# Performance work log

Hardware: AMD Instinct MI355X
Metric: run time of the kernel (lower is better)

The kernel has to match this reference:

```python
import jax, jax.numpy as jnp
import numpy as np

NPOINT = 1024
NSAMPLE = 32
BN_EPS = 1e-5


def setup_inputs() -> dict:
    key = jax.random.key(0)
    ks = jax.random.split(key, 8)
    B, N, C = 16, 4096, 64
    chans = [C + 3, 64, 64, 128]
    d = {
        "xyz": jax.random.normal(ks[0], (B, N, 3), jnp.float32),
        "points": jax.random.normal(ks[1], (B, N, C), jnp.float32),
    }
    for i in range(3):
        d[f"w{i+1}"] = jax.random.normal(ks[2 + i], (chans[i + 1], chans[i]), jnp.float32) / np.sqrt(chans[i]).astype(np.float32)
        d[f"b{i+1}"] = jnp.zeros((chans[i + 1],), jnp.float32)
        d[f"g{i+1}"] = jnp.ones((chans[i + 1],), jnp.float32)
        d[f"be{i+1}"] = jnp.zeros((chans[i + 1],), jnp.float32)
    return d


def farthest_point_sample(xyz, npoint):
    # xyz: [B, N, 3] -> centroids: [B, npoint] int32 (deterministic start at index 0)
    B, N, _ = xyz.shape

    def step(carry, _):
        distance, farthest = carry
        centroid = jnp.take_along_axis(xyz, farthest[:, None, None], axis=1)  # [B,1,3]
        dist = jnp.sum((xyz - centroid) ** 2, axis=-1)                         # [B,N]
        distance = jnp.minimum(distance, dist)
        new_far = jnp.argmax(distance, axis=-1).astype(jnp.int32)
        return (distance, new_far), farthest

    init = (jnp.full((B, N), 1e10, xyz.dtype), jnp.zeros((B,), jnp.int32))
    _, cents = jax.lax.scan(step, init, None, length=npoint)  # [npoint, B]
    return cents.T  # [B, npoint]


def index_points(points, idx):
    # points: [B,N,C], idx: [B,...] -> [B,...,C]
    return jax.vmap(lambda p, i: p[i])(points, idx)


def bn_relu(h, g, be):
    # training-mode BatchNorm over all axes except channel (last), biased var
    m = h.mean(axis=(0, 1, 2), keepdims=True)
    v = h.var(axis=(0, 1, 2), keepdims=True)
    return jax.nn.relu((h - m) / jnp.sqrt(v + BN_EPS) * g + be)


def reference(xyz, points, w1, b1, g1, be1, w2, b2, g2, be2, w3, b3, g3, be3):
    # --- sample_and_group ---
    fps_idx = farthest_point_sample(xyz, NPOINT)           # [B,S]
    new_xyz = index_points(xyz, fps_idx)                   # [B,S,3]
    # query_ball_point in source ignores radius: kNN via argsort of sq dists
    sqrdists = jnp.sum((new_xyz[:, :, None, :] - xyz[:, None, :, :]) ** 2, axis=-1)  # [B,S,N]
    _, group_idx = jax.lax.top_k(-sqrdists, NSAMPLE)       # [B,S,K] smallest distances
    grouped_xyz = index_points(xyz, group_idx) - new_xyz[:, :, None, :]  # [B,S,K,3]
    grouped_pts = index_points(points, group_idx)          # [B,S,K,C]
    new_points = jnp.concatenate([grouped_xyz, grouped_pts], axis=-1)    # [B,S,K,C+3]
    # --- shared MLP (1x1 conv + BN + ReLU) x3, channel-last layout ---
    h = bn_relu(jnp.einsum("bskc,oc->bsko", new_points, w1) + b1, g1, be1)
    h = bn_relu(jnp.einsum("bskc,oc->bsko", h, w2) + b2, g2, be2)
    h = bn_relu(jnp.einsum("bskc,oc->bsko", h, w3) + b3, g3, be3)
    # max-pool over the neighbor (nsample) axis
    out = jnp.max(h, axis=2)  # [B,S,128]
    return (new_xyz, out)
```

## Files before the change

### kernel.cpp

```cpp
#include <hip/hip_runtime.h>
#include <cstdint>

#define NB   16
#define NPT  4096
#define CINP 64
#define SP   1024
#define KNB  32
#define NROWS (NB*SP*KNB)
#define NT_F  524288.0f
#define NBLK12 4096
#define NBLK3  8192

typedef float v2f __attribute__((ext_vector_type(2)));

__device__ __forceinline__ float sqdist3(float ax, float ay, float az,
                                         float bx, float by, float bz) {
  float dx = ax - bx, dy = ay - by, dz = az - bz;
  return __fadd_rn(__fadd_rn(__fmul_rn(dx, dx), __fmul_rn(dy, dy)), __fmul_rn(dz, dz));
}

#define DPP_STAGE_MAXF(v, ctrl)                                                   \
  do {                                                                            \
    int _t = __builtin_amdgcn_update_dpp(0, __float_as_int(v), ctrl, 0xf, 0xf, false); \
    v = fmaxf(v, __int_as_float(_t));                                             \
  } while (0)

__device__ __forceinline__ float wave_max_f32(float v) {
  DPP_STAGE_MAXF(v, 0x111);
  DPP_STAGE_MAXF(v, 0x112);
  DPP_STAGE_MAXF(v, 0x114);
  DPP_STAGE_MAXF(v, 0x118);
  DPP_STAGE_MAXF(v, 0x142);
  DPP_STAGE_MAXF(v, 0x143);
  return __int_as_float(__builtin_amdgcn_readlane(__float_as_int(v), 63));
}

#define DPP_STAGE_MINU(v, ctrl)                                                   \
  do {                                                                            \
    unsigned _t = (unsigned)__builtin_amdgcn_update_dpp(                          \
        (int)0xFFFFFFFF, (int)(v), ctrl, 0xf, 0xf, false);                        \
    v = (v < _t) ? v : _t;                                                        \
  } while (0)

__device__ __forceinline__ unsigned wave_min_u32(unsigned v) {
  DPP_STAGE_MINU(v, 0x111);
  DPP_STAGE_MINU(v, 0x112);
  DPP_STAGE_MINU(v, 0x114);
  DPP_STAGE_MINU(v, 0x118);
  DPP_STAGE_MINU(v, 0x142);
  DPP_STAGE_MINU(v, 0x143);
  return (unsigned)__builtin_amdgcn_readlane((int)v, 63);
}

#define DPP_STAGE_ADDI(v, ctrl)                                                   \
  do {                                                                            \
    int _t = __builtin_amdgcn_update_dpp(0, (v), ctrl, 0xf, 0xf, false);          \
    v += _t;                                                                      \
  } while (0)

__device__ __forceinline__ int wave_sum_i32(int v) {
  DPP_STAGE_ADDI(v, 0x111);
  DPP_STAGE_ADDI(v, 0x112);
  DPP_STAGE_ADDI(v, 0x114);
  DPP_STAGE_ADDI(v, 0x118);
  DPP_STAGE_ADDI(v, 0x142);
  DPP_STAGE_ADDI(v, 0x143);
  return __builtin_amdgcn_readlane(v, 63);
}

__global__ __launch_bounds__(256) void fps_kernel(const float* __restrict__ xyz,
                                                  float* __restrict__ newxyz) {
#pragma clang fp contract(off)
  const int b = blockIdx.x, t = threadIdx.x;
  __shared__ __align__(16) float s4[NPT * 4];
  __shared__ unsigned long long s_red[2][4];
  const float* gx = xyz + b * NPT * 3;
  for (int i = t; i < NPT * 3; i += 256) s4[(i / 3) * 4 + (i % 3)] = gx[i];
  __syncthreads();
  v2f px[8], py[8], pz[8], dst[8];
#pragma unroll
  for (int k = 0; k < 8; ++k) {
    float4 a = *(const float4*)&s4[(t + (2 * k) * 256) * 4];
    float4 c = *(const float4*)&s4[(t + (2 * k + 1) * 256) * 4];
    px[k].x = a.x; px[k].y = c.x;
    py[k].x = a.y; py[k].y = c.y;
    pz[k].x = a.z; pz[k].y = c.z;
    dst[k].x = 1e10f; dst[k].y = 1e10f;
  }
  float cx = s4[0], cy = s4[1], cz = s4[2];
  const int w = t >> 6;
  int buf = 0;
  for (int it = 0; it < SP; ++it) {
    if (t == 0) {
      float* o = newxyz + (b * SP + it) * 3;
      o[0] = cx; o[1] = cy; o[2] = cz;
    }
    v2f vcx; vcx.x = cx; vcx.y = cx;
    v2f vcy; vcy.x = cy; vcy.y = cy;
    v2f vcz; vcz.x = cz; vcz.y = cz;
    float bd = -1.0f; int bi = 0;
#pragma unroll
    for (int k = 0; k < 8; ++k) {
      v2f dx = px[k] - vcx;
      v2f dy = py[k] - vcy;
      v2f dz = pz[k] - vcz;
      v2f dd = (dx * dx + dy * dy) + dz * dz;
      float n0 = fminf(dst[k].x, dd.x);
      float n1 = fminf(dst[k].y, dd.y);
      dst[k].x = n0; dst[k].y = n1;
      if (n0 > bd) { bd = n0; bi = t + (2 * k) * 256; }
      if (n1 > bd) { bd = n1; bi = t + (2 * k + 1) * 256; }
    }
    float dw = wave_max_f32(bd);
    unsigned cand = (bd == dw) ? (unsigned)bi : 0xFFFFFFFFu;
    unsigned iw = wave_min_u32(cand);
    if ((t & 63) == 0)
      s_red[buf][w] = ((unsigned long long)__float_as_uint(dw) << 32) | (4095u - iw);
    __syncthreads();
    unsigned long long k0 = s_red[buf][0], k1 = s_red[buf][1];
    unsigned long long k2 = s_red[buf][2], k3 = s_red[buf][3];
    unsigned long long ka = k0 > k1 ? k0 : k1;
    unsigned long long kb = k2 > k3 ? k2 : k3;
    unsigned long long km = ka > kb ? ka : kb;
    int p = 4095 - (int)(km & 0xFFFFFFFFull);
    float4 cc = *(const float4*)&s4[p * 4];
    cx = cc.x; cy = cc.y; cz = cc.z;
    buf ^= 1;
  }
}

__global__ __launch_bounds__(256) void knn_kernel(const float* __restrict__ xyz,
                                                  const float* __restrict__ newxyz,
                                                  int* __restrict__ gidx) {
  const int t = threadIdx.x, lane = t & 63, w = t >> 6;
  const int q = blockIdx.x * 4 + w;
  const int b = q >> 10;
  const float* nx = newxyz + q * 3;
  const float qx = nx[0], qy = nx[1], qz = nx[2];
  const float* xb = xyz + b * NPT * 3;
  float d[64];
#pragma unroll
  for (int j = 0; j < 64; ++j) {
    int p = j * 64 + lane;
    d[j] = sqdist3(xb[p * 3], xb[p * 3 + 1], xb[p * 3 + 2], qx, qy, qz);
  }
  unsigned V = 0;
  for (int bit = 30; bit >= 0; --bit) {
    unsigned cand = V | (1u << bit);
    int c = 0;
#pragma unroll
    for (int j = 0; j < 64; ++j) c += (__float_as_uint(d[j]) < cand) ? 1 : 0;
    int ct = wave_sum_i32(c);
    if (ct < KNB) V = cand;
  }
  __shared__ int s_cnt[4], s_eqcnt[4], s_eq[4][64];
  if (lane == 0) { s_cnt[w] = 0; s_eqcnt[w] = 0; }
  __syncthreads();
  int* gout = gidx + q * KNB;
#pragma unroll
  for (int j = 0; j < 64; ++j) {
    unsigned db = __float_as_uint(d[j]);
    if (db < V) {
      int pos = atomicAdd(&s_cnt[w], 1);
      if (pos < KNB) gout[pos] = j * 64 + lane;
    } else if (db == V) {
      int pos = atomicAdd(&s_eqcnt[w], 1);
      if (pos < 64) s_eq[w][pos] = j * 64 + lane;
    }
  }
  __syncthreads();
  if (lane == 0) {
    int c1 = s_cnt[w]; if (c1 > KNB) c1 = KNB;
    int ne = s_eqcnt[w]; if (ne > 64) ne = 64;
    int need = KNB - c1;
    for (int m = 0; m < need; ++m) {
      int bi = -1, bv = 0x7fffffff;
      for (int e = 0; e < ne; ++e) {
        int v = s_eq[w][e];
        if (v < bv) { bv = v; bi = e; }
      }
      gout[c1 + m] = bv;
      if (bi >= 0) s_eq[w][bi] = 0x7fffffff;
    }
  }
}

__global__ __launch_bounds__(256) void layer1_kernel(
    const float* __restrict__ xyz, const float* __restrict__ points,
    const float* __restrict__ newxyz, const int* __restrict__ gidx,
    const float* __restrict__ w1, const float* __restrict__ b1,
    float* __restrict__ h1, float* __restrict__ part) {
  const int t = threadIdx.x, blk = blockIdx.x;
  const int R0 = blk * 128;
  const int b = R0 >> 15;
  __shared__ __align__(16) float xs[67][132];
  __shared__ __align__(16) float wsm[67][68];
  __shared__ float red[2][32][64];
  {
    int o = t & 63;
    for (int c = t >> 6; c < 67; c += 4) wsm[c][o] = w1[o * 67 + c];
  }
  {
    int r = t >> 1, q = t & 1;
    int R = R0 + r;
    int idx = gidx[R];
    if (q == 0) {
      const float* xp = xyz + (size_t)(b * NPT + idx) * 3;
      const float* nq = newxyz + (size_t)(R >> 5) * 3;
      xs[0][r] = xp[0] - nq[0];
      xs[1][r] = xp[1] - nq[1];
      xs[2][r] = xp[2] - nq[2];
    }
    const float* pp = points + (size_t)(b * NPT + idx) * CINP + q * 32;
#pragma unroll
    for (int i = 0; i < 8; ++i) {
      float4 v = *(const float4*)(pp + i * 4);
      int c = 3 + q * 32 + i * 4;
      xs[c][r] = v.x; xs[c + 1][r] = v.y; xs[c + 2][r] = v.z; xs[c + 3][r] = v.w;
    }
  }
  __syncthreads();
  const int tr = t & 31, to = t >> 5;
  float acc[4][8];
#pragma unroll
  for (int j = 0; j < 8; ++j) {
    float bb = b1[to * 8 + j];
#pragma unroll
    for (int i = 0; i < 4; ++i) acc[i][j] = bb;
  }
  for (int c = 0; c < 67; ++c) {
    float4 xv = *(const float4*)&xs[c][tr * 4];
    float4 w0 = *(const float4*)&wsm[c][to * 8];
    float4 w1v = *(const float4*)&wsm[c][to * 8 + 4];
    float xa[4] = {xv.x, xv.y, xv.z, xv.w};
    float wa[8] = {w0.x, w0.y, w0.z, w0.w, w1v.x, w1v.y, w1v.z, w1v.w};
#pragma unroll
    for (int i = 0; i < 4; ++i)
#pragma unroll
      for (int j = 0; j < 8; ++j) acc[i][j] += xa[i] * wa[j];
  }
#pragma unroll
  for (int i = 0; i < 4; ++i) {
    float4 s0; s0.x = acc[i][0]; s0.y = acc[i][1]; s0.z = acc[i][2]; s0.w = acc[i][3];
    float4 s1; s1.x = acc[i][4]; s1.y = acc[i][5]; s1.z = acc[i][6]; s1.w = acc[i][7];
    float* hp = &h1[(size_t)(R0 + tr * 4 + i) * 64 + to * 8];
    *(float4*)hp = s0;
    *(float4*)(hp + 4) = s1;
  }
#pragma unroll
  for (int j = 0; j < 8; ++j) {
    float s1 = acc[0][j] + acc[1][j] + acc[2][j] + acc[3][j];
    float s2 = acc[0][j] * acc[0][j] + acc[1][j] * acc[1][j] +
               acc[2][j] * acc[2][j] + acc[3][j] * acc[3][j];
    red[0][tr][to * 8 + j] = s1;
    red[1][tr][to * 8 + j] = s2;
  }
  __syncthreads();
  if (t < 128) {
    int stat = t >> 6, o = t & 63;
    float v = 0.f;
#pragma unroll
    for (int k = 0; k < 32; ++k) v += red[stat][k][o];
    part[(size_t)(stat * 64 + o) * NBLK12 + blk] = v;
  }
}

__global__ __launch_bounds__(256) void layer2_kernel(
    const float* __restrict__ hin, const float* __restrict__ bn,
    const float* __restrict__ w2, const float* __restrict__ b2,
    float* __restrict__ hout, float* __restrict__ part) {
  const int t = threadIdx.x, blk = blockIdx.x;
  const size_t R0 = (size_t)blk * 128;
  __shared__ __align__(16) float xs[64][132];
  __shared__ __align__(16) float wsm[64][68];
  __shared__ float red[2][32][64];
  {
    int o = t & 63;
    for (int c = t >> 6; c < 64; c += 4) wsm[c][o] = w2[o * 64 + c];
  }
  {
    int r = t >> 1, q = t & 1;
    const float* hp = hin + (R0 + r) * 64 + q * 32;
#pragma unroll
    for (int i = 0; i < 8; ++i) {
      int c = q * 32 + i * 4;
      float4 v = *(const float4*)(hp + i * 4);
      float4 sc = *(const float4*)(bn + c);
      float4 sh = *(const float4*)(bn + 64 + c);
      xs[c][r]     = fmaxf(v.x * sc.x + sh.x, 0.f);
      xs[c + 1][r] = fmaxf(v.y * sc.y + sh.y, 0.f);
      xs[c + 2][r] = fmaxf(v.z * sc.z + sh.z, 0.f);
      xs[c + 3][r] = fmaxf(v.w * sc.w + sh.w, 0.f);
    }
  }
  __syncthreads();
  const int tr = t & 31, to = t >> 5;
  float acc[4][8];
#pragma unroll
  for (int j = 0; j < 8; ++j) {
    float bb = b2[to * 8 + j];
#pragma unroll
    for (int i = 0; i < 4; ++i) acc[i][j] = bb;
  }
  for (int c = 0; c < 64; ++c) {
    float4 xv = *(const float4*)&xs[c][tr * 4];
    float4 w0 = *(const float4*)&wsm[c][to * 8];
    float4 w1v = *(const float4*)&wsm[c][to * 8 + 4];
    float xa[4] = {xv.x, xv.y, xv.z, xv.w};
    float wa[8] = {w0.x, w0.y, w0.z, w0.w, w1v.x, w1v.y, w1v.z, w1v.w};
#pragma unroll
    for (int i = 0; i < 4; ++i)
#pragma unroll
      for (int j = 0; j < 8; ++j) acc[i][j] += xa[i] * wa[j];
  }
#pragma unroll
  for (int i = 0; i < 4; ++i) {
    float4 s0; s0.x = acc[i][0]; s0.y = acc[i][1]; s0.z = acc[i][2]; s0.w = acc[i][3];
    float4 s1; s1.x = acc[i][4]; s1.y = acc[i][5]; s1.z = acc[i][6]; s1.w = acc[i][7];
    float* hp = &hout[(R0 + tr * 4 + i) * 64 + to * 8];
    *(float4*)hp = s0;
    *(float4*)(hp + 4) = s1;
  }
#pragma unroll
  for (int j = 0; j < 8; ++j) {
    float s1 = acc[0][j] + acc[1][j] + acc[2][j] + acc[3][j];
    float s2 = acc[0][j] * acc[0][j] + acc[1][j] * acc[1][j] +
               acc[2][j] * acc[2][j] + acc[3][j] * acc[3][j];
    red[0][tr][to * 8 + j] = s1;
    red[1][tr][to * 8 + j] = s2;
  }
  __syncthreads();
  if (t < 128) {
    int stat = t >> 6, o = t & 63;
    float v = 0.f;
#pragma unroll
    for (int k = 0; k < 32; ++k) v += red[stat][k][o];
    part[(size_t)(stat * 64 + o) * NBLK12 + blk] = v;
  }
}

__global__ __launch_bounds__(256) void layer3_kernel(
    const float* __restrict__ hin, const float* __restrict__ bn,
    const float* __restrict__ w3, const float* __restrict__ b3,
    float* __restrict__ maxh, float* __restrict__ minh, float* __restrict__ part) {
  const int t = threadIdx.x, blk = blockIdx.x;
  const size_t R0 = (size_t)blk * 64;
  __shared__ __align__(16) float smem[64 * 68 + 64 * 136];
  float* xs = smem;
  float* wsm = smem + 64 * 68;
  {
    int o = t & 127, q = t >> 7;
    for (int c = q; c < 64; c += 2) wsm[c * 136 + o] = w3[o * 64 + c];
  }
  {
    int r = t >> 2, q = t & 3;
    const float* hp = hin + (R0 + r) * 64 + q * 16;
#pragma unroll
    for (int i = 0; i < 4; ++i) {
      int c = q * 16 + i * 4;
      float4 v = *(const float4*)(hp + i * 4);
      float4 sc = *(const float4*)(bn + c);
      float4 sh = *(const float4*)(bn + 64 + c);
      xs[c * 68 + r]       = fmaxf(v.x * sc.x + sh.x, 0.f);
      xs[(c + 1) * 68 + r] = fmaxf(v.y * sc.y + sh.y, 0.f);
      xs[(c + 2) * 68 + r] = fmaxf(v.z * sc.z + sh.z, 0.f);
      xs[(c + 3) * 68 + r] = fmaxf(v.w * sc.w + sh.w, 0.f);
    }
  }
  __syncthreads();
  const int tr = t & 15, to = t >> 4;
  float acc[4][8];
#pragma unroll
  for (int j = 0; j < 8; ++j) {
    float bb = b3[to * 8 + j];
#pragma unroll
    for (int i = 0; i < 4; ++i) acc[i][j] = bb;
  }
  for (int c = 0; c < 64; ++c) {
    float4 xv = *(const float4*)&xs[c * 68 + tr * 4];
    float4 wv0 = *(const float4*)&wsm[c * 136 + to * 8];
    float4 wv1 = *(const float4*)&wsm[c * 136 + to * 8 + 4];
    float xa[4] = {xv.x, xv.y, xv.z, xv.w};
    float wa[8] = {wv0.x, wv0.y, wv0.z, wv0.w, wv1.x, wv1.y, wv1.z, wv1.w};
#pragma unroll
    for (int i = 0; i < 4; ++i)
#pragma unroll
      for (int j = 0; j < 8; ++j) acc[i][j] += xa[i] * wa[j];
  }
  __syncthreads();
  float* red = smem;
#pragma unroll
  for (int j = 0; j < 8; ++j) {
    float s1 = acc[0][j] + acc[1][j] + acc[2][j] + acc[3][j];
    float s2 = acc[0][j] * acc[0][j] + acc[1][j] * acc[1][j] +
               acc[2][j] * acc[2][j] + acc[3][j] * acc[3][j];
    red[(0 * 16 + tr) * 128 + to * 8 + j] = s1;
    red[(1 * 16 + tr) * 128 + to * 8 + j] = s2;
  }
  __syncthreads();
  {
    int stat = t >> 7, o = t & 127;
    float v = 0.f;
#pragma unroll
    for (int k = 0; k < 16; ++k) v += red[(stat * 16 + k) * 128 + o];
    part[(size_t)(stat * 128 + o) * NBLK3 + blk] = v;
  }
  __syncthreads();
#pragma unroll
  for (int j = 0; j < 8; ++j) {
    float mx = fmaxf(fmaxf(acc[0][j], acc[1][j]), fmaxf(acc[2][j], acc[3][j]));
    float mn = fminf(fminf(acc[0][j], acc[1][j]), fminf(acc[2][j], acc[3][j]));
    red[(0 * 16 + tr) * 128 + to * 8 + j] = mx;
    red[(1 * 16 + tr) * 128 + to * 8 + j] = mn;
  }
  __syncthreads();
  {
    int g = t >> 7, o = t & 127;
    float mx = -1e30f, mn = 1e30f;
#pragma unroll
    for (int k = 0; k < 8; ++k) {
      mx = fmaxf(mx, red[(0 * 16 + g * 8 + k) * 128 + o]);
      mn = fminf(mn, red[(1 * 16 + g * 8 + k) * 128 + o]);
    }
    size_t bs = (size_t)blk * 2 + g;
    maxh[bs * 128 + o] = mx;
    minh[bs * 128 + o] = mn;
  }
}

__global__ __launch_bounds__(256) void bn_finalize(const float* __restrict__ part,
                                                   const float* __restrict__ g,
                                                   const float* __restrict__ be,
                                                   float* __restrict__ bnout,
                                                   int Cout, int nblk) {
  const int o = blockIdx.x, t = threadIdx.x;
  float s1 = 0.f, s2 = 0.f;
  const float* p1 = part + (size_t)o * nblk;
  const float* p2 = part + (size_t)(Cout + o) * nblk;
  for (int i = t; i < nblk; i += 256) { s1 += p1[i]; s2 += p2[i]; }
#pragma unroll
  for (int off = 32; off >= 1; off >>= 1) {
    s1 += __shfl_xor(s1, off);
    s2 += __shfl_xor(s2, off);
  }
  __shared__ float r1[4], r2[4];
  if ((t & 63) == 0) { r1[t >> 6] = s1; r2[t >> 6] = s2; }
  __syncthreads();
  if (t == 0) {
    float S1 = r1[0] + r1[1] + r1[2] + r1[3];
    float S2 = r2[0] + r2[1] + r2[2] + r2[3];
    float m = S1 / NT_F;
    float v = S2 / NT_F - m * m;
    if (v < 0.f) v = 0.f;
    float inv = 1.0f / sqrtf(v + 1e-5f);
    float sc = g[o] * inv;
    bnout[o] = sc;
    bnout[Cout + o] = be[o] - m * sc;
  }
}

__global__ __launch_bounds__(256) void finalize_kernel(const float* __restrict__ maxh,
                                                       const float* __restrict__ minh,
                                                       const float* __restrict__ bn,
                                                       float* __restrict__ out2) {
  int i = blockIdx.x * 256 + threadIdx.x;
  int o = i & 127;
  float sc = bn[o], sh = bn[128 + o];
  float a = sc * maxh[i] + sh;
  float c = sc * minh[i] + sh;
  out2[i] = fmaxf(fmaxf(a, c), 0.f);
}

extern "C" void kernel_launch(void* const* d_in, const int* in_sizes, int n_in,
                              void* d_out, int out_size, void* d_ws, size_t ws_size,
                              hipStream_t stream) {
  const float* xyz = (const float*)d_in[0];
  const float* points = (const float*)d_in[1];
  const float* w1 = (const float*)d_in[2];
  const float* b1 = (const float*)d_in[3];
  const float* g1 = (const float*)d_in[4];
  const float* be1 = (const float*)d_in[5];
  const float* w2 = (const float*)d_in[6];
  const float* b2 = (const float*)d_in[7];
  const float* g2 = (const float*)d_in[8];
  const float* be2 = (const float*)d_in[9];
  const float* w3 = (const float*)d_in[10];
  const float* b3 = (const float*)d_in[11];
  const float* g3 = (const float*)d_in[12];
  const float* be3 = (const float*)d_in[13];

  float* out = (float*)d_out;
  float* newxyz = out;
  float* out2 = out + 49152;

  const size_t MiB = 1u << 20;
  char* wsb = (char*)d_ws;
  int*   gidx = (int*)wsb;
  float* h    = (float*)(wsb + 2 * MiB);
  float* part = (float*)(wsb + 130 * MiB);
  float* maxh = (float*)(wsb + 138 * MiB);
  float* minh = (float*)(wsb + 146 * MiB);
  float* bn1  = (float*)(wsb + 154 * MiB);
  float* bn2  = bn1 + 128;
  float* bn3  = bn2 + 128;

  hipLaunchKernelGGL(fps_kernel, dim3(NB), dim3(256), 0, stream, xyz, newxyz);
  hipLaunchKernelGGL(knn_kernel, dim3(16384 / 4), dim3(256), 0, stream, xyz, newxyz, gidx);
  hipLaunchKernelGGL(layer1_kernel, dim3(NBLK12), dim3(256), 0, stream,
                     xyz, points, newxyz, gidx, w1, b1, h, part);
  hipLaunchKernelGGL(bn_finalize, dim3(64), dim3(256), 0, stream, part, g1, be1, bn1, 64, NBLK12);
  hipLaunchKernelGGL(layer2_kernel, dim3(NBLK12), dim3(256), 0, stream, h, bn1, w2, b2, h, part);
  hipLaunchKernelGGL(bn_finalize, dim3(64), dim3(256), 0, stream, part, g2, be2, bn2, 64, NBLK12);
  hipLaunchKernelGGL(layer3_kernel, dim3(NBLK3), dim3(256), 0, stream,
                     h, bn2, w3, b3, maxh, minh, part);
  hipLaunchKernelGGL(bn_finalize, dim3(128), dim3(256), 0, stream, part, g3, be3, bn3, 128, NBLK3);
  hipLaunchKernelGGL(finalize_kernel, dim3(2097152 / 256), dim3(256), 0, stream,
                     maxh, minh, bn3, out2);
}
```

Measured before the change: 1.336 ms.

## Replace FPS barrier with tagged LDS spin-wait and transpose BN partial layout

In farthest point sampling, the per-iteration __syncthreads is replaced by a tag-based spin wait on volatile LDS slots. The wave argmin reduction becomes a ballot plus readlane, and points are assigned contiguously per thread so the lowest index still wins ties. The BN partial sums are stored block-major (row per block) and the reduce kernel reads them that way. Shared reduction arrays are padded to avoid bank conflicts. The restrict qualifiers on the aliased h buffer are dropped. The spin wait relies on waves making forward progress and on LDS ordering without a fence, and the strided partial reads in the reduce kernel may be less coalesced.

```diff
diff --git a/kernel.cpp b/kernel.cpp
--- a/kernel.cpp
+++ b/kernel.cpp
@@ -35,23 +35,6 @@
   return __int_as_float(__builtin_amdgcn_readlane(__float_as_int(v), 63));
 }
 
-#define DPP_STAGE_MINU(v, ctrl)                                                   \
-  do {                                                                            \
-    unsigned _t = (unsigned)__builtin_amdgcn_update_dpp(                          \
-        (int)0xFFFFFFFF, (int)(v), ctrl, 0xf, 0xf, false);                        \
-    v = (v < _t) ? v : _t;                                                        \
-  } while (0)
-
-__device__ __forceinline__ unsigned wave_min_u32(unsigned v) {
-  DPP_STAGE_MINU(v, 0x111);
-  DPP_STAGE_MINU(v, 0x112);
-  DPP_STAGE_MINU(v, 0x114);
-  DPP_STAGE_MINU(v, 0x118);
-  DPP_STAGE_MINU(v, 0x142);
-  DPP_STAGE_MINU(v, 0x143);
-  return (unsigned)__builtin_amdgcn_readlane((int)v, 63);
-}
-
 #define DPP_STAGE_ADDI(v, ctrl)                                                   \
   do {                                                                            \
     int _t = __builtin_amdgcn_update_dpp(0, (v), ctrl, 0xf, 0xf, false);          \
@@ -73,15 +56,19 @@
 #pragma clang fp contract(off)
   const int b = blockIdx.x, t = threadIdx.x;
   __shared__ __align__(16) float s4[NPT * 4];
-  __shared__ unsigned long long s_red[2][4];
+  __shared__ unsigned s_tag[2][4], s_hi[2][4], s_lo[2][4];
+  volatile unsigned* vtag = &s_tag[0][0];
+  volatile unsigned* vhi  = &s_hi[0][0];
+  volatile unsigned* vlo  = &s_lo[0][0];
   const float* gx = xyz + b * NPT * 3;
   for (int i = t; i < NPT * 3; i += 256) s4[(i / 3) * 4 + (i % 3)] = gx[i];
+  if (t < 8) s_tag[t >> 2][t & 3] = 0xFFFFFFFFu;
   __syncthreads();
   v2f px[8], py[8], pz[8], dst[8];
 #pragma unroll
   for (int k = 0; k < 8; ++k) {
-    float4 a = *(const float4*)&s4[(t + (2 * k) * 256) * 4];
-    float4 c = *(const float4*)&s4[(t + (2 * k + 1) * 256) * 4];
+    float4 a = *(const float4*)&s4[(t * 16 + 2 * k) * 4];
+    float4 c = *(const float4*)&s4[(t * 16 + 2 * k + 1) * 4];
     px[k].x = a.x; px[k].y = c.x;
     py[k].x = a.y; py[k].y = c.y;
     pz[k].x = a.z; pz[k].y = c.z;
@@ -108,21 +95,32 @@
       float n0 = fminf(dst[k].x, dd.x);
       float n1 = fminf(dst[k].y, dd.y);
       dst[k].x = n0; dst[k].y = n1;
-      if (n0 > bd) { bd = n0; bi = t + (2 * k) * 256; }
-      if (n1 > bd) { bd = n1; bi = t + (2 * k + 1) * 256; }
+      if (n0 > bd) { bd = n0; bi = t * 16 + 2 * k; }
+      if (n1 > bd) { bd = n1; bi = t * 16 + 2 * k + 1; }
     }
     float dw = wave_max_f32(bd);
-    unsigned cand = (bd == dw) ? (unsigned)bi : 0xFFFFFFFFu;
-    unsigned iw = wave_min_u32(cand);
-    if ((t & 63) == 0)
-      s_red[buf][w] = ((unsigned long long)__float_as_uint(dw) << 32) | (4095u - iw);
-    __syncthreads();
-    unsigned long long k0 = s_red[buf][0], k1 = s_red[buf][1];
-    unsigned long long k2 = s_red[buf][2], k3 = s_red[buf][3];
+    unsigned long long mask = __ballot(bd == dw);
+    int wl = __ffsll(mask) - 1;
+    unsigned iw = (unsigned)__builtin_amdgcn_readlane(bi, wl);
+    if ((t & 63) == 0) {
+      vhi[buf * 4 + w] = __float_as_uint(dw);
+      vlo[buf * 4 + w] = 4095u - iw;
+      vtag[buf * 4 + w] = (unsigned)it;
+    }
+    for (;;) {
+      unsigned t0 = vtag[buf * 4 + 0], t1 = vtag[buf * 4 + 1];
+      unsigned t2 = vtag[buf * 4 + 2], t3 = vtag[buf * 4 + 3];
+      if (t0 == (unsigned)it && t1 == (unsigned)it &&
+          t2 == (unsigned)it && t3 == (unsigned)it) break;
+    }
+    unsigned long long k0 = ((unsigned long long)vhi[buf * 4 + 0] << 32) | vlo[buf * 4 + 0];
+    unsigned long long k1 = ((unsigned long long)vhi[buf * 4 + 1] << 32) | vlo[buf * 4 + 1];
+    unsigned long long k2 = ((unsigned long long)vhi[buf * 4 + 2] << 32) | vlo[buf * 4 + 2];
+    unsigned long long k3 = ((unsigned long long)vhi[buf * 4 + 3] << 32) | vlo[buf * 4 + 3];
     unsigned long long ka = k0 > k1 ? k0 : k1;
     unsigned long long kb = k2 > k3 ? k2 : k3;
     unsigned long long km = ka > kb ? ka : kb;
-    int p = 4095 - (int)(km & 0xFFFFFFFFull);
+    int p = 4095 - (int)(km & 0xFFFull);
     float4 cc = *(const float4*)&s4[p * 4];
     cx = cc.x; cy = cc.y; cz = cc.z;
     buf ^= 1;
@@ -195,7 +193,7 @@
   const int b = R0 >> 15;
   __shared__ __align__(16) float xs[67][132];
   __shared__ __align__(16) float wsm[67][68];
-  __shared__ float red[2][32][64];
+  __shared__ float red[2][32][65];
   {
     int o = t & 63;
     for (int c = t >> 6; c < 67; c += 4) wsm[c][o] = w1[o * 67 + c];
@@ -261,19 +259,19 @@
     float v = 0.f;
 #pragma unroll
     for (int k = 0; k < 32; ++k) v += red[stat][k][o];
-    part[(size_t)(stat * 64 + o) * NBLK12 + blk] = v;
+    part[(size_t)blk * 128 + t] = v;
   }
 }
 
 __global__ __launch_bounds__(256) void layer2_kernel(
-    const float* __restrict__ hin, const float* __restrict__ bn,
+    const float* hin, const float* __restrict__ bn,
     const float* __restrict__ w2, const float* __restrict__ b2,
-    float* __restrict__ hout, float* __restrict__ part) {
+    float* hout, float* __restrict__ part) {
   const int t = threadIdx.x, blk = blockIdx.x;
   const size_t R0 = (size_t)blk * 128;
   __shared__ __align__(16) float xs[64][132];
   __shared__ __align__(16) float wsm[64][68];
-  __shared__ float red[2][32][64];
+  __shared__ float red[2][32][65];
   {
     int o = t & 63;
     for (int c = t >> 6; c < 64; c += 4) wsm[c][o] = w2[o * 64 + c];
@@ -335,7 +333,7 @@
     float v = 0.f;
 #pragma unroll
     for (int k = 0; k < 32; ++k) v += red[stat][k][o];
-    part[(size_t)(stat * 64 + o) * NBLK12 + blk] = v;
+    part[(size_t)blk * 128 + t] = v;
   }
 }
 
@@ -394,24 +392,24 @@
     float s1 = acc[0][j] + acc[1][j] + acc[2][j] + acc[3][j];
     float s2 = acc[0][j] * acc[0][j] + acc[1][j] * acc[1][j] +
                acc[2][j] * acc[2][j] + acc[3][j] * acc[3][j];
-    red[(0 * 16 + tr) * 128 + to * 8 + j] = s1;
-    red[(1 * 16 + tr) * 128 + to * 8 + j] = s2;
+    red[(0 * 16 + tr) * 129 + to * 8 + j] = s1;
+    red[(1 * 16 + tr) * 129 + to * 8 + j] = s2;
   }
   __syncthreads();
   {
     int stat = t >> 7, o = t & 127;
     float v = 0.f;
 #pragma unroll
-    for (int k = 0; k < 16; ++k) v += red[(stat * 16 + k) * 128 + o];
-    part[(size_t)(stat * 128 + o) * NBLK3 + blk] = v;
+    for (int k = 0; k < 16; ++k) v += red[(stat * 16 + k) * 129 + o];
+    part[(size_t)blk * 256 + t] = v;
   }
   __syncthreads();
 #pragma unroll
   for (int j = 0; j < 8; ++j) {
     float mx = fmaxf(fmaxf(acc[0][j], acc[1][j]), fmaxf(acc[2][j], acc[3][j]));
     float mn = fminf(fminf(acc[0][j], acc[1][j]), fminf(acc[2][j], acc[3][j]));
-    red[(0 * 16 + tr) * 128 + to * 8 + j] = mx;
-    red[(1 * 16 + tr) * 128 + to * 8 + j] = mn;
+    red[(0 * 16 + tr) * 129 + to * 8 + j] = mx;
+    red[(1 * 16 + tr) * 129 + to * 8 + j] = mn;
   }
   __syncthreads();
   {
@@ -419,8 +417,8 @@
     float mx = -1e30f, mn = 1e30f;
 #pragma unroll
     for (int k = 0; k < 8; ++k) {
-      mx = fmaxf(mx, red[(0 * 16 + g * 8 + k) * 128 + o]);
-      mn = fminf(mn, red[(1 * 16 + g * 8 + k) * 128 + o]);
+      mx = fmaxf(mx, red[(0 * 16 + g * 8 + k) * 129 + o]);
+      mn = fminf(mn, red[(1 * 16 + g * 8 + k) * 129 + o]);
     }
     size_t bs = (size_t)blk * 2 + g;
     maxh[bs * 128 + o] = mx;
@@ -428,16 +426,19 @@
   }
 }
 
-__global__ __launch_bounds__(256) void bn_finalize(const float* __restrict__ part,
-                                                   const float* __restrict__ g,
-                                                   const float* __restrict__ be,
-                                                   float* __restrict__ bnout,
-                                                   int Cout, int nblk) {
+__global__ __launch_bounds__(256) void bn_reduce(const float* __restrict__ part,
+                                                 const float* __restrict__ g,
+                                                 const float* __restrict__ be,
+                                                 float* __restrict__ bnout,
+                                                 int Cout, int nblk) {
   const int o = blockIdx.x, t = threadIdx.x;
+  const int row = 2 * Cout;
   float s1 = 0.f, s2 = 0.f;
-  const float* p1 = part + (size_t)o * nblk;
-  const float* p2 = part + (size_t)(Cout + o) * nblk;
-  for (int i = t; i < nblk; i += 256) { s1 += p1[i]; s2 += p2[i]; }
+  for (int r = t; r < nblk; r += 256) {
+    const float* p = part + (size_t)r * row;
+    s1 += p[o];
+    s2 += p[Cout + o];
+  }
 #pragma unroll
   for (int off = 32; off >= 1; off >>= 1) {
     s1 += __shfl_xor(s1, off);
@@ -496,24 +497,24 @@
   const size_t MiB = 1u << 20;
   char* wsb = (char*)d_ws;
   int*   gidx = (int*)wsb;
+  float* bn1  = (float*)(wsb + 1 * MiB);
+  float* bn2  = bn1 + 256;
+  float* bn3  = bn2 + 256;
   float* h    = (float*)(wsb + 2 * MiB);
   float* part = (float*)(wsb + 130 * MiB);
   float* maxh = (float*)(wsb + 138 * MiB);
   float* minh = (float*)(wsb + 146 * MiB);
-  float* bn1  = (float*)(wsb + 154 * MiB);
-  float* bn2  = bn1 + 128;
-  float* bn3  = bn2 + 128;
 
   hipLaunchKernelGGL(fps_kernel, dim3(NB), dim3(256), 0, stream, xyz, newxyz);
   hipLaunchKernelGGL(knn_kernel, dim3(16384 / 4), dim3(256), 0, stream, xyz, newxyz, gidx);
   hipLaunchKernelGGL(layer1_kernel, dim3(NBLK12), dim3(256), 0, stream,
                      xyz, points, newxyz, gidx, w1, b1, h, part);
-  hipLaunchKernelGGL(bn_finalize, dim3(64), dim3(256), 0, stream, part, g1, be1, bn1, 64, NBLK12);
+  hipLaunchKernelGGL(bn_reduce, dim3(64), dim3(256), 0, stream, part, g1, be1, bn1, 64, NBLK12);
   hipLaunchKernelGGL(layer2_kernel, dim3(NBLK12), dim3(256), 0, stream, h, bn1, w2, b2, h, part);
-  hipLaunchKernelGGL(bn_finalize, dim3(64), dim3(256), 0, stream, part, g2, be2, bn2, 64, NBLK12);
+  hipLaunchKernelGGL(bn_reduce, dim3(64), dim3(256), 0, stream, part, g2, be2, bn2, 64, NBLK12);
   hipLaunchKernelGGL(layer3_kernel, dim3(NBLK3), dim3(256), 0, stream,
                      h, bn2, w3, b3, maxh, minh, part);
-  hipLaunchKernelGGL(bn_finalize, dim3(128), dim3(256), 0, stream, part, g3, be3, bn3, 128, NBLK3);
+  hipLaunchKernelGGL(bn_reduce, dim3(128), dim3(256), 0, stream, part, g3, be3, bn3, 128, NBLK3);
   hipLaunchKernelGGL(finalize_kernel, dim3(2097152 / 256), dim3(256), 0, stream,
                      maxh, minh, bn3, out2);
 }
```

After: 1.767 ms. 32.3% more time.
